# Kernel tuning notes

Hardware: AMD Instinct MI355X
Metric: run time of the kernel (lower is better)

Reference implementation:

```python
import jax, jax.numpy as jnp
import numpy as np

DIM = 576
HEADS = 8
AGENT = 49
GRID_SIZE = 5
ORDER = 3
BN_EPS = 1e-5


def _kan_grid():
    h = 2.0 / GRID_SIZE  # grid_range [-1, 1]
    return jnp.arange(-ORDER, GRID_SIZE + ORDER + 1, dtype=jnp.float32) * h - 1.0


def _bsplines(x, grid):
    # x: (M, in) -> (M, in, GRID_SIZE + ORDER) Cox-de Boor B-spline bases (efficient-kan)
    xe = x[..., None]
    b = ((xe >= grid[:-1]) & (xe < grid[1:])).astype(x.dtype)
    for k in range(1, ORDER + 1):
        b = ((xe - grid[:-(k + 1)]) / (grid[k:-1] - grid[:-(k + 1)]) * b[..., :-1]
             + (grid[k + 1:] - xe) / (grid[k + 1:] - grid[1:-k]) * b[..., 1:])
    return b


def setup_inputs() -> dict:
    key = jax.random.key(0)
    ks = jax.random.split(key, 16)
    b, H, W = 32, 28, 28
    n, c = H * W, DIM
    nrm = lambda k, shape, std=0.02: jax.random.normal(k, shape, jnp.float32) * std
    return {
        "x": jax.random.normal(ks[0], (b, n, c), jnp.float32),
        "H": H,
        "W": W,
        "Wq": nrm(ks[1], (c, c)),
        "Wkv": nrm(ks[2], (2 * c, c)),
        "an_bias": nrm(ks[3], (HEADS, AGENT, 7, 7)),
        "na_bias": nrm(ks[4], (HEADS, AGENT, 7, 7)),
        "ah_bias": nrm(ks[5], (1, HEADS, AGENT, H, 1)),
        "aw_bias": nrm(ks[6], (1, HEADS, AGENT, 1, W)),
        "ha_bias": nrm(ks[7], (1, HEADS, H, 1, AGENT)),
        "wa_bias": nrm(ks[8], (1, HEADS, 1, W, AGENT)),
        "dwc_w": nrm(ks[9], (c, 1, 3, 3), 0.1),
        "dwc_b": jnp.zeros((c,), jnp.float32),
        "bn_gamma": jnp.ones((c,), jnp.float32),
        "bn_beta": jnp.zeros((c,), jnp.float32),
        "bn_mean": jnp.zeros((c,), jnp.float32),
        "bn_var": jnp.ones((c,), jnp.float32),
        "base_weight": nrm(ks[10], (c, c)),
        "spline_weight": nrm(ks[11], (c, c, GRID_SIZE + ORDER)),
        "spline_scaler": jnp.ones((c, c), jnp.float32),
    }


def reference(x, H, W, Wq, Wkv, an_bias, na_bias, ah_bias, aw_bias, ha_bias, wa_bias,
              dwc_w, dwc_b, bn_gamma, bn_beta, bn_mean, bn_var,
              base_weight, spline_weight, spline_scaler):
    b, n, c = x.shape
    h, hd = HEADS, c // HEADS
    scale = hd ** -0.5
    q = x @ Wq.T                       # (b,n,c)
    kv = x @ Wkv.T                     # (b,n,2c)  (sr_ratio == 1)
    k, v = kv[..., :c], kv[..., c:]
    # agent tokens: AdaptiveAvgPool2d(28x28 -> 7x7) == exact 4x4 mean pooling
    p = int(AGENT ** 0.5)
    agent = q.reshape(b, p, H // p, p, W // p, c).mean(axis=(2, 4)).reshape(b, AGENT, c)
    qh = q.reshape(b, n, h, hd).transpose(0, 2, 1, 3)       # (b,h,n,hd)
    kh = k.reshape(b, n, h, hd).transpose(0, 2, 1, 3)
    vh = v.reshape(b, n, h, hd).transpose(0, 2, 1, 3)
    ah = agent.reshape(b, AGENT, h, hd).transpose(0, 2, 1, 3)  # (b,h,A,hd)
    # stage 1: agent tokens attend to k/v (bilinear-upsampled 7x7 bias + separable bias)
    pb1 = jax.image.resize(an_bias, (h, AGENT, H, W), "bilinear").reshape(1, h, AGENT, n)
    pb2 = (ah_bias + aw_bias).reshape(1, h, AGENT, n)
    agent_attn = jax.nn.softmax(jnp.einsum("bhad,bhnd->bhan", ah * scale, kh) + pb1 + pb2, axis=-1)
    agent_v = jnp.einsum("bhan,bhnd->bhad", agent_attn, vh)    # (b,h,A,hd)
    # stage 2: queries attend to agent tokens
    ab1 = jax.image.resize(na_bias, (h, AGENT, H, W), "bilinear").reshape(1, h, AGENT, n).transpose(0, 1, 3, 2)
    ab2 = (ha_bias + wa_bias).reshape(1, h, n, AGENT)
    q_attn = jax.nn.softmax(jnp.einsum("bhnd,bhad->bhna", qh * scale, ah) + ab1 + ab2, axis=-1)
    out = jnp.einsum("bhna,bhad->bhnd", q_attn, agent_v).transpose(0, 2, 1, 3).reshape(b, n, c)
    # depthwise-conv + BN(eval) + ReLU residual on v
    vimg = v.transpose(0, 2, 1).reshape(b, c, H, W)
    y = jax.lax.conv_general_dilated(vimg, dwc_w, (1, 1), "SAME",
                                     feature_group_count=c,
                                     dimension_numbers=("NCHW", "OIHW", "NCHW"))
    y = y + dwc_b[None, :, None, None]
    scale_bn = (bn_gamma / jnp.sqrt(bn_var + BN_EPS))[None, :, None, None]
    y = (y - bn_mean[None, :, None, None]) * scale_bn + bn_beta[None, :, None, None]
    y = jax.nn.relu(y).reshape(b, c, n).transpose(0, 2, 1)
    out = out + y
    # KANLinear projection: silu base branch + B-spline branch
    xf = out.reshape(b * n, c)
    bases = _bsplines(xf, _kan_grid())                           # (M, in, 8)
    scaled = spline_weight * spline_scaler[..., None]            # (out, in, 8)
    proj = jax.nn.silu(xf) @ base_weight.T + jnp.einsum("mik,oik->mo", bases, scaled)
    return proj.reshape(b, n, c)
```

## Files before the change

### kernel.cpp

```cpp
#include <hip/hip_runtime.h>
#include <hip/hip_bf16.h>
#include <math.h>

#define B_ 32
#define N_ 784
#define C_ 576
#define H_ 28
#define W_ 28
#define HEADS_ 8
#define HD_ 72
#define AGENT_ 49
#define M_ (B_ * N_)
#define KTOT_ 5184
#define QKVW_ 1728
#define SCALE_ 0.11785113019775793f
#define LDA_ 40

typedef unsigned short ushort_t;
typedef __attribute__((ext_vector_type(8))) unsigned short u16x8;
typedef __attribute__((ext_vector_type(8))) __bf16 bf16x8;
typedef __attribute__((ext_vector_type(4))) float f32x4;
typedef __attribute__((ext_vector_type(4))) unsigned u32x4;

__device__ __forceinline__ ushort_t f2bf(float f) {
  union { float f; unsigned u; } v; v.f = f;
  unsigned r = v.u + 0x7fffu + ((v.u >> 16) & 1u);
  return (ushort_t)(r >> 16);
}
__device__ __forceinline__ float bf2f(ushort_t u) {
  union { unsigned u; float f; } v; v.u = ((unsigned)u) << 16;
  return v.f;
}
__device__ __forceinline__ unsigned pack2(float lo, float hi) {
  __bf16 a = (__bf16)lo, b = (__bf16)hi;
  unsigned short ua = __builtin_bit_cast(unsigned short, a);
  unsigned short ub = __builtin_bit_cast(unsigned short, b);
  return (unsigned)ua | ((unsigned)ub << 16);
}

__global__ __launch_bounds__(256) void convert_x_kernel(
    const float* __restrict__ x, ushort_t* __restrict__ xbf) {
  const int total8 = M_ * C_ / 8;
  for (int i = blockIdx.x * 256 + threadIdx.x; i < total8; i += gridDim.x * 256) {
    f32x4 a = *(const f32x4*)(x + i * 8);
    f32x4 b = *(const f32x4*)(x + i * 8 + 4);
    u16x8 o;
    o[0]=f2bf(a[0]); o[1]=f2bf(a[1]); o[2]=f2bf(a[2]); o[3]=f2bf(a[3]);
    o[4]=f2bf(b[0]); o[5]=f2bf(b[1]); o[6]=f2bf(b[2]); o[7]=f2bf(b[3]);
    *(u16x8*)(xbf + i * 8) = o;
  }
}

__global__ __launch_bounds__(256) void pack_w_kernel(
    const float* __restrict__ Wq, const float* __restrict__ Wkv,
    ushort_t* __restrict__ wbf) {
  int total = QKVW_ * C_;
  for (int i = blockIdx.x * 256 + threadIdx.x; i < total; i += gridDim.x * 256) {
    int j = i / C_, k = i % C_;
    float v = (j < C_) ? Wq[(size_t)j * C_ + k] : Wkv[(size_t)(j - C_) * C_ + k];
    wbf[i] = f2bf(v);
  }
}

__global__ __launch_bounds__(256) void pack_b_kernel(
    const float* __restrict__ base_w, const float* __restrict__ spline_w,
    const float* __restrict__ spline_s, ushort_t* __restrict__ bpackb) {
  int o = blockIdx.x;
  for (int j = threadIdx.x; j < KTOT_; j += 256) {
    float v;
    if (j < C_) {
      v = base_w[(size_t)o * C_ + j];
    } else {
      int jj = j - C_;
      int i = jj >> 3, kk = jj & 7;
      v = spline_w[((size_t)o * C_ + i) * 8 + kk] * spline_s[(size_t)o * C_ + i];
    }
    bpackb[(size_t)o * KTOT_ + j] = f2bf(v);
  }
}

__device__ __forceinline__ float bilerp7(const float* __restrict__ Bsrc, int y, int x) {
  float sy = y * 0.25f - 0.375f;
  float sx = x * 0.25f - 0.375f;
  float fy0 = floorf(sy), fx0 = floorf(sx);
  int y0 = (int)fy0, x0 = (int)fx0;
  float fy = sy - fy0, fx = sx - fx0;
  int y0c = min(6, max(0, y0)), y1c = min(6, max(0, y0 + 1));
  int x0c = min(6, max(0, x0)), x1c = min(6, max(0, x0 + 1));
  float v00 = Bsrc[y0c * 7 + x0c], v01 = Bsrc[y0c * 7 + x1c];
  float v10 = Bsrc[y1c * 7 + x0c], v11 = Bsrc[y1c * 7 + x1c];
  return (1.f - fy) * ((1.f - fx) * v00 + fx * v01)
       + fy * ((1.f - fx) * v10 + fx * v11);
}

__global__ __launch_bounds__(256) void bias_kernel(
    const float* __restrict__ an_bias, const float* __restrict__ na_bias,
    const float* __restrict__ ah_bias, const float* __restrict__ aw_bias,
    const float* __restrict__ ha_bias, const float* __restrict__ wa_bias,
    float* __restrict__ abias, float* __restrict__ qbias) {
  int idx = blockIdx.x * 256 + threadIdx.x;
  if (idx >= HEADS_ * AGENT_ * N_) return;
  int n = idx % N_;
  int ha = idx / N_;
  int h = ha / AGENT_, a = ha % AGENT_;
  int y = n / W_, x = n % W_;
  float pb1 = bilerp7(an_bias + (size_t)ha * 49, y, x);
  float pb2 = ah_bias[ha * H_ + y] + aw_bias[ha * W_ + x];
  abias[(size_t)ha * N_ + n] = pb1 + pb2;
  float ab1 = bilerp7(na_bias + (size_t)ha * 49, y, x);
  float ab2 = ha_bias[(h * H_ + y) * AGENT_ + a] + wa_bias[(h * W_ + x) * AGENT_ + a];
  qbias[((size_t)h * N_ + n) * AGENT_ + a] = ab1 + ab2;
}

__global__ __launch_bounds__(256, 2) void mfma_qkv_kernel(
    const ushort_t* __restrict__ A, const ushort_t* __restrict__ Bt,
    ushort_t* __restrict__ out) {
  __shared__ ushort_t Asl[2][128 * LDA_];
  __shared__ ushort_t Bsl[2][192 * LDA_];
  const int tid = threadIdx.x;
  const int lane = tid & 63, wid = tid >> 6;
  const int wm = wid >> 1, wn = wid & 1;
  const int m0 = blockIdx.y * 128, n0 = blockIdx.x * 192;
  const int l16 = lane & 15, lq = lane >> 4;

  const int rA = tid >> 1, hA = tid & 1;
  int rB[3], cB[3];
  #pragma unroll
  for (int u = 0; u < 3; ++u) { int it = tid + u * 256; rB[u] = it >> 2; cB[u] = it & 3; }

  const ushort_t* arow = A + (size_t)(m0 + rA) * C_ + hA * 16;

  f32x4 acc[4][6] = {};
  u16x8 ar0, ar1, br[3];

  ar0 = *(const u16x8*)(arow + 0);
  ar1 = *(const u16x8*)(arow + 8);
  #pragma unroll
  for (int u = 0; u < 3; ++u)
    br[u] = *(const u16x8*)(Bt + (size_t)(n0 + rB[u]) * C_ + cB[u] * 8);
  *(u16x8*)&Asl[0][rA * LDA_ + hA * 16] = ar0;
  *(u16x8*)&Asl[0][rA * LDA_ + hA * 16 + 8] = ar1;
  #pragma unroll
  for (int u = 0; u < 3; ++u) *(u16x8*)&Bsl[0][rB[u] * LDA_ + cB[u] * 8] = br[u];
  ar0 = *(const u16x8*)(arow + 32);
  ar1 = *(const u16x8*)(arow + 40);
  #pragma unroll
  for (int u = 0; u < 3; ++u)
    br[u] = *(const u16x8*)(Bt + (size_t)(n0 + rB[u]) * C_ + 32 + cB[u] * 8);
  __syncthreads();

  const int NSTEP = C_ / 32;
  for (int s = 0; s < NSTEP; ++s) {
    const int cur = s & 1;
    bf16x8 af[4], bfr[6];
    #pragma unroll
    for (int fm = 0; fm < 4; ++fm)
      af[fm] = *(const bf16x8*)&Asl[cur][(wm * 64 + fm * 16 + l16) * LDA_ + lq * 8];
    #pragma unroll
    for (int fn = 0; fn < 6; ++fn)
      bfr[fn] = *(const bf16x8*)&Bsl[cur][(wn * 96 + fn * 16 + l16) * LDA_ + lq * 8];
    #pragma unroll
    for (int fm = 0; fm < 4; ++fm)
      #pragma unroll
      for (int fn = 0; fn < 6; ++fn)
        acc[fm][fn] = __builtin_amdgcn_mfma_f32_16x16x32_bf16(
            af[fm], bfr[fn], acc[fm][fn], 0, 0, 0);
    if (s + 1 < NSTEP) {
      const int nxt = cur ^ 1;
      *(u16x8*)&Asl[nxt][rA * LDA_ + hA * 16] = ar0;
      *(u16x8*)&Asl[nxt][rA * LDA_ + hA * 16 + 8] = ar1;
      #pragma unroll
      for (int u = 0; u < 3; ++u) *(u16x8*)&Bsl[nxt][rB[u] * LDA_ + cB[u] * 8] = br[u];
      if (s + 2 < NSTEP) {
        const int kl = (s + 2) * 32;
        ar0 = *(const u16x8*)(arow + kl);
        ar1 = *(const u16x8*)(arow + kl + 8);
        #pragma unroll
        for (int u = 0; u < 3; ++u)
          br[u] = *(const u16x8*)(Bt + (size_t)(n0 + rB[u]) * C_ + kl + cB[u] * 8);
      }
    }
    __syncthreads();
  }
  #pragma unroll
  for (int fm = 0; fm < 4; ++fm) {
    #pragma unroll
    for (int fn = 0; fn < 6; ++fn) {
      int col = n0 + wn * 96 + fn * 16 + l16;
      #pragma unroll
      for (int r = 0; r < 4; ++r) {
        int row = m0 + wm * 64 + fm * 16 + lq * 4 + r;
        out[(size_t)row * QKVW_ + col] = f2bf(acc[fm][fn][r]);
      }
    }
  }
}

__device__ __forceinline__ u32x4 basesPack(float xv) {
  float s = __fmaf_rn(xv, 2.5f, 5.5f);
  float tf = floorf(s);
  int t = (int)tf;
  float u = s - tf;
  float u2 = u * u, u3 = u2 * u, um = 1.f - u;
  float p0 = u3 * (1.f / 6.f);
  float p1 = (-3.f * u3 + 3.f * u2 + 3.f * u + 1.f) * (1.f / 6.f);
  float p2 = (3.f * u3 - 6.f * u2 + 4.f) * (1.f / 6.f);
  float p3 = um * um * um * (1.f / 6.f);
  unsigned lo = pack2(p3, p2);
  unsigned hi = pack2(p1, p0);
  unsigned cm1 = lo << 16;
  unsigned c1  = (lo >> 16) | (hi << 16);
  unsigned c3  = hi >> 16;
  bool inr = (t >= 0) && (t <= 10);
  u32x4 o;
  #pragma unroll
  for (int j = 0; j < 4; ++j) {
    int d = 3 - t + 2 * j;
    unsigned r = 0u;
    r = (d == -1) ? cm1 : r;
    r = (d == 0)  ? lo  : r;
    r = (d == 1)  ? c1  : r;
    r = (d == 2)  ? hi  : r;
    r = (d == 3)  ? c3  : r;
    o[j] = inr ? r : 0u;
  }
  return o;
}

__device__ __forceinline__ u32x4 siluPack(const float* xv) {
  u32x4 o;
  #pragma unroll
  for (int e = 0; e < 4; ++e) {
    float v0 = xv[2 * e], v1 = xv[2 * e + 1];
    float s0 = v0 / (1.f + __expf(-v0));
    float s1 = v1 / (1.f + __expf(-v1));
    o[e] = pack2(s0, s1);
  }
  return o;
}

__global__ __launch_bounds__(256, 2) void kan_mfma_kernel(
    const float* __restrict__ xf, const ushort_t* __restrict__ Bt,
    float* __restrict__ out) {
  __shared__ ushort_t Asl[2][128 * LDA_];
  __shared__ ushort_t Bsl[2][192 * LDA_];
  const int tid = threadIdx.x;
  const int lane = tid & 63, wid = tid >> 6;
  const int wm = wid >> 1, wn = wid & 1;
  const int m0 = blockIdx.y * 128, n0 = blockIdx.x * 192;
  const int l16 = lane & 15, lq = lane >> 4;

  const int rA = tid >> 1, hA = tid & 1;
  int rB[3], cB[3];
  #pragma unroll
  for (int u = 0; u < 3; ++u) { int it = tid + u * 256; rB[u] = it >> 2; cB[u] = it & 3; }

  const float* xfr = xf + (size_t)(m0 + rA) * C_;

  f32x4 acc[4][6] = {};
  float xv[16];
  u16x8 br[3];

  #pragma unroll
  for (int q = 0; q < 4; ++q) {
    f32x4 t4 = *(const f32x4*)(xfr + hA * 16 + q * 4);
    xv[q * 4 + 0] = t4[0]; xv[q * 4 + 1] = t4[1];
    xv[q * 4 + 2] = t4[2]; xv[q * 4 + 3] = t4[3];
  }
  #pragma unroll
  for (int u = 0; u < 3; ++u)
    br[u] = *(const u16x8*)(Bt + (size_t)(n0 + rB[u]) * KTOT_ + cB[u] * 8);
  {
    u32x4 a0 = siluPack(xv), a1 = siluPack(xv + 8);
    *(u32x4*)&Asl[0][rA * LDA_ + hA * 16] = a0;
    *(u32x4*)&Asl[0][rA * LDA_ + hA * 16 + 8] = a1;
    #pragma unroll
    for (int u = 0; u < 3; ++u) *(u16x8*)&Bsl[0][rB[u] * LDA_ + cB[u] * 8] = br[u];
  }
  #pragma unroll
  for (int q = 0; q < 4; ++q) {
    f32x4 t4 = *(const f32x4*)(xfr + 32 + hA * 16 + q * 4);
    xv[q * 4 + 0] = t4[0]; xv[q * 4 + 1] = t4[1];
    xv[q * 4 + 2] = t4[2]; xv[q * 4 + 3] = t4[3];
  }
  #pragma unroll
  for (int u = 0; u < 3; ++u)
    br[u] = *(const u16x8*)(Bt + (size_t)(n0 + rB[u]) * KTOT_ + 32 + cB[u] * 8);
  __syncthreads();

  const int NSTEP = KTOT_ / 32;
  for (int s = 0; s < NSTEP; ++s) {
    const int cur = s & 1;
    bf16x8 af[4], bfr[6];
    #pragma unroll
    for (int fm = 0; fm < 4; ++fm)
      af[fm] = *(const bf16x8*)&Asl[cur][(wm * 64 + fm * 16 + l16) * LDA_ + lq * 8];
    #pragma unroll
    for (int fn = 0; fn < 6; ++fn)
      bfr[fn] = *(const bf16x8*)&Bsl[cur][(wn * 96 + fn * 16 + l16) * LDA_ + lq * 8];
    #pragma unroll
    for (int fm = 0; fm < 4; ++fm)
      #pragma unroll
      for (int fn = 0; fn < 6; ++fn)
        acc[fm][fn] = __builtin_amdgcn_mfma_f32_16x16x32_bf16(
            af[fm], bfr[fn], acc[fm][fn], 0, 0, 0);
    if (s + 1 < NSTEP) {
      const int nxt = cur ^ 1;
      const int kg = (s + 1) * 32;
      u32x4 a0, a1;
      if (kg < C_) { a0 = siluPack(xv); a1 = siluPack(xv + 8); }
      else         { a0 = basesPack(xv[0]); a1 = basesPack(xv[1]); }
      *(u32x4*)&Asl[nxt][rA * LDA_ + hA * 16] = a0;
      *(u32x4*)&Asl[nxt][rA * LDA_ + hA * 16 + 8] = a1;
      #pragma unroll
      for (int u = 0; u < 3; ++u) *(u16x8*)&Bsl[nxt][rB[u] * LDA_ + cB[u] * 8] = br[u];
      if (s + 2 < NSTEP) {
        const int kl = (s + 2) * 32;
        if (kl < C_) {
          #pragma unroll
          for (int q = 0; q < 4; ++q) {
            f32x4 t4 = *(const f32x4*)(xfr + kl + hA * 16 + q * 4);
            xv[q * 4 + 0] = t4[0]; xv[q * 4 + 1] = t4[1];
            xv[q * 4 + 2] = t4[2]; xv[q * 4 + 3] = t4[3];
          }
        } else {
          int i0 = ((kl - C_) >> 3) + hA * 2;
          xv[0] = xfr[i0];
          xv[1] = xfr[i0 + 1];
        }
        #pragma unroll
        for (int u = 0; u < 3; ++u)
          br[u] = *(const u16x8*)(Bt + (size_t)(n0 + rB[u]) * KTOT_ + kl + cB[u] * 8);
      }
    }
    __syncthreads();
  }
  #pragma unroll
  for (int fm = 0; fm < 4; ++fm) {
    #pragma unroll
    for (int fn = 0; fn < 6; ++fn) {
      int col = n0 + wn * 96 + fn * 16 + l16;
      #pragma unroll
      for (int r = 0; r < 4; ++r) {
        int row = m0 + wm * 64 + fm * 16 + lq * 4 + r;
        out[(size_t)row * C_ + col] = acc[fm][fn][r];
      }
    }
  }
}

__global__ __launch_bounds__(576) void agent_pool_kernel(
    const ushort_t* __restrict__ qkvb, float* __restrict__ agent) {
  int ba = blockIdx.x;
  int b = ba / AGENT_, a = ba % AGENT_;
  int ay = a / 7, ax = a % 7;
  int ch = threadIdx.x;
  float s = 0.f;
  #pragma unroll
  for (int i2 = 0; i2 < 4; ++i2)
    #pragma unroll
    for (int i4 = 0; i4 < 4; ++i4)
      s += bf2f(qkvb[((size_t)b * N_ + (ay * 4 + i2) * W_ + (ax * 4 + i4)) * QKVW_ + ch]);
  agent[(size_t)ba * C_ + ch] = s * 0.0625f;
}

#define AKS_ 104
#define VTS_ 136
__global__ __launch_bounds__(256) void agent_attn_mfma_kernel(
    const float* __restrict__ agent, const ushort_t* __restrict__ qkvb,
    const float* __restrict__ abias, float* __restrict__ agent_v) {
  __shared__ ushort_t A_lds[64 * AKS_];
  __shared__ ushort_t K_lds[112 * AKS_];
  __shared__ ushort_t Vt_lds[80 * VTS_];
  __shared__ ushort_t P_lds[4][16 * VTS_];
  const int tid = threadIdx.x;
  const int lane = tid & 63, wid = tid >> 6;
  const int l16 = lane & 15, lq = lane >> 4;
  const int b = blockIdx.x >> 3, h = blockIdx.x & 7;

  for (int i = tid; i < 64 * AKS_; i += 256) A_lds[i] = 0;
  for (int i = tid; i < 112 * 32; i += 256) {
    int r = i >> 5, cc = 72 + (i & 31);
    K_lds[r * AKS_ + cc] = 0;
  }
  for (int i = tid; i < 80 * VTS_; i += 256) Vt_lds[i] = 0;
  for (int i = tid; i < 4 * 16 * 24; i += 256) {
    int w = i / (16 * 24), rest = i % (16 * 24);
    int r = rest / 24, cc = 112 + rest % 24;
    P_lds[w][r * VTS_ + cc] = 0;
  }
  for (int i = tid; i < AGENT_ * HD_; i += 256) {
    int a = i / HD_, d = i % HD_;
    A_lds[a * AKS_ + d] = f2bf(agent[((size_t)b * AGENT_ + a) * C_ + h * HD_ + d]);
  }

  int srow[4], scol[4]; bool sval[4];
  #pragma unroll
  for (int i = 0; i < 4; ++i) {
    int idx = tid + i * 256;
    srow[i] = idx / 9; scol[i] = idx % 9;
    sval[i] = idx < 1008;
  }
  const ushort_t* kbase = qkvb + (size_t)b * N_ * QKVW_ + C_ + h * HD_;
  const ushort_t* vbase = qkvb + (size_t)b * N_ * QKVW_ + 2 * C_ + h * HD_;

  u16x8 kreg[4], vreg[4];
  #pragma unroll
  for (int i = 0; i < 4; ++i) {
    if (sval[i]) {
      kreg[i] = *(const u16x8*)(kbase + (size_t)srow[i] * QKVW_ + scol[i] * 8);
      vreg[i] = *(const u16x8*)(vbase + (size_t)srow[i] * QKVW_ + scol[i] * 8);
    }
  }
  #pragma unroll
  for (int i = 0; i < 4; ++i) {
    if (sval[i]) {
      *(u16x8*)&K_lds[srow[i] * AKS_ + scol[i] * 8] = kreg[i];
      #pragma unroll
      for (int e = 0; e < 8; ++e)
        Vt_lds[(scol[i] * 8 + e) * VTS_ + srow[i]] = vreg[i][e];
    }
  }
  __syncthreads();

  float m_r[4] = {-1e30f, -1e30f, -1e30f, -1e30f};
  float l_r[4] = {};
  f32x4 O[5] = {};
  const float* bias_base[4];
  #pragma unroll
  for (int r = 0; r < 4; ++r) {
    int a = wid * 16 + lq * 4 + r;
    a = min(a, AGENT_ - 1);
    bias_base[r] = abias + ((size_t)h * AGENT_ + a) * N_;
  }

  for (int c = 0; c < 7; ++c) {
    if (c < 6) {
      const size_t off = (size_t)(c + 1) * 112 * QKVW_;
      #pragma unroll
      for (int i = 0; i < 4; ++i) {
        if (sval[i]) {
          kreg[i] = *(const u16x8*)(kbase + off + (size_t)srow[i] * QKVW_ + scol[i] * 8);
          vreg[i] = *(const u16x8*)(vbase + off + (size_t)srow[i] * QKVW_ + scol[i] * 8);
        }
      }
    }
    f32x4 sacc[7] = {};
    #pragma unroll
    for (int ks = 0; ks < 3; ++ks) {
      bf16x8 af = *(const bf16x8*)&A_lds[(wid * 16 + l16) * AKS_ + ks * 32 + lq * 8];
      #pragma unroll
      for (int nt = 0; nt < 7; ++nt) {
        bf16x8 bf = *(const bf16x8*)&K_lds[(nt * 16 + l16) * AKS_ + ks * 32 + lq * 8];
        sacc[nt] = __builtin_amdgcn_mfma_f32_16x16x32_bf16(af, bf, sacc[nt], 0, 0, 0);
      }
    }
    float cmax[4] = {-1e30f, -1e30f, -1e30f, -1e30f};
    const int nb = c * 112 + l16;
    #pragma unroll
    for (int nt = 0; nt < 7; ++nt)
      #pragma unroll
      for (int r = 0; r < 4; ++r) {
        float lg = sacc[nt][r] * SCALE_ + bias_base[r][nb + nt * 16];
        sacc[nt][r] = lg;
        cmax[r] = fmaxf(cmax[r], lg);
      }
    #pragma unroll
    for (int off = 1; off < 16; off <<= 1)
      #pragma unroll
      for (int r = 0; r < 4; ++r)
        cmax[r] = fmaxf(cmax[r], __shfl_xor(cmax[r], off));
    float scl[4], rs[4];
    #pragma unroll
    for (int r = 0; r < 4; ++r) {
      float nm = fmaxf(m_r[r], cmax[r]);
      scl[r] = __expf(m_r[r] - nm);
      m_r[r] = nm;
      rs[r] = 0.f;
    }
    #pragma unroll
    for (int nt = 0; nt < 7; ++nt)
      #pragma unroll
      for (int r = 0; r < 4; ++r) {
        float p = __expf(sacc[nt][r] - m_r[r]);
        rs[r] += p;
        P_lds[wid][(lq * 4 + r) * VTS_ + nt * 16 + l16] = f2bf(p);
      }
    #pragma unroll
    for (int off = 1; off < 16; off <<= 1)
      #pragma unroll
      for (int r = 0; r < 4; ++r)
        rs[r] += __shfl_xor(rs[r], off);
    #pragma unroll
    for (int r = 0; r < 4; ++r) l_r[r] = l_r[r] * scl[r] + rs[r];
    #pragma unroll
    for (int nt = 0; nt < 5; ++nt)
      #pragma unroll
      for (int r = 0; r < 4; ++r) O[nt][r] *= scl[r];
    #pragma unroll
    for (int ks = 0; ks < 4; ++ks) {
      bf16x8 pf = *(const bf16x8*)&P_lds[wid][l16 * VTS_ + ks * 32 + lq * 8];
      #pragma unroll
      for (int nt = 0; nt < 5; ++nt) {
        bf16x8 vf = *(const bf16x8*)&Vt_lds[(nt * 16 + l16) * VTS_ + ks * 32 + lq * 8];
        O[nt] = __builtin_amdgcn_mfma_f32_16x16x32_bf16(pf, vf, O[nt], 0, 0, 0);
      }
    }
    __syncthreads();
    if (c < 6) {
      #pragma unroll
      for (int i = 0; i < 4; ++i) {
        if (sval[i]) {
          *(u16x8*)&K_lds[srow[i] * AKS_ + scol[i] * 8] = kreg[i];
          #pragma unroll
          for (int e = 0; e < 8; ++e)
            Vt_lds[(scol[i] * 8 + e) * VTS_ + srow[i]] = vreg[i][e];
        }
      }
      __syncthreads();
    }
  }
  float inv[4];
  #pragma unroll
  for (int r = 0; r < 4; ++r) inv[r] = 1.f / l_r[r];
  #pragma unroll
  for (int nt = 0; nt < 5; ++nt) {
    int d = nt * 16 + l16;
    if (d >= HD_) continue;
    #pragma unroll
    for (int r = 0; r < 4; ++r) {
      int a = wid * 16 + lq * 4 + r;
      if (a < AGENT_)
        agent_v[(((size_t)b * HEADS_ + h) * AGENT_ + a) * HD_ + d] = O[nt][r] * inv[r];
    }
  }
}

__global__ __launch_bounds__(256) void q_attn_kernel(
    const ushort_t* __restrict__ qkvb, const float* __restrict__ agent,
    const float* __restrict__ agent_v, const float* __restrict__ qbias,
    float* __restrict__ xf) {
  __shared__ float ag_t[HD_ * 52];
  __shared__ float av_t[HD_ * 52];
  const int tid = threadIdx.x;
  const int h = blockIdx.y, b = blockIdx.z;
  for (int t = tid; t < AGENT_ * HD_; t += 256) {
    int a = t / HD_, d = t % HD_;
    ag_t[d * 52 + a] = agent[((size_t)b * AGENT_ + a) * C_ + h * HD_ + d];
    av_t[d * 52 + a] = agent_v[(((size_t)b * HEADS_ + h) * AGENT_ + a) * HD_ + d];
  }
  __syncthreads();
  const int n = blockIdx.x * 256 + tid;
  if (n >= N_) return;
  const ushort_t* qp = qkvb + ((size_t)b * N_ + n) * QKVW_ + h * HD_;
  const float* qb = qbias + ((size_t)h * N_ + n) * AGENT_;
  float lg[AGENT_];
  #pragma unroll
  for (int a = 0; a < AGENT_; ++a) lg[a] = qb[a];
  for (int d = 0; d < HD_; ++d) {
    float qd = bf2f(qp[d]) * SCALE_;
    #pragma unroll
    for (int a = 0; a < AGENT_; ++a) lg[a] += qd * ag_t[d * 52 + a];
  }
  float mx = -1e30f;
  #pragma unroll
  for (int a = 0; a < AGENT_; ++a) mx = fmaxf(mx, lg[a]);
  float s = 0.f;
  #pragma unroll
  for (int a = 0; a < AGENT_; ++a) { lg[a] = __expf(lg[a] - mx); s += lg[a]; }
  float inv = 1.f / s;
  #pragma unroll
  for (int a = 0; a < AGENT_; ++a) lg[a] *= inv;
  float* op = xf + ((size_t)b * N_ + n) * C_ + h * HD_;
  for (int d = 0; d < HD_; ++d) {
    float acc = 0.f;
    #pragma unroll
    for (int a = 0; a < AGENT_; ++a) acc += lg[a] * av_t[d * 52 + a];
    op[d] = acc;
  }
}

__global__ __launch_bounds__(288) void dwc_kernel(
    const ushort_t* __restrict__ qkvb, const float* __restrict__ w,
    const float* __restrict__ bias, const float* __restrict__ gamma,
    const float* __restrict__ beta, const float* __restrict__ mean,
    const float* __restrict__ var, float* __restrict__ xf) {
  const int bn = blockIdx.x;
  const int b = bn / N_, n = bn % N_;
  const int y = n / W_, x = n % W_;
  const int c0 = threadIdx.x * 2;
  float a0 = 0.f, a1 = 0.f;
  #pragma unroll
  for (int ky = 0; ky < 3; ++ky) {
    int yy = y + ky - 1;
    if (yy < 0 || yy >= H_) continue;
    #pragma unroll
    for (int kx = 0; kx < 3; ++kx) {
      int xx = x + kx - 1;
      if (xx < 0 || xx >= W_) continue;
      unsigned v = *(const unsigned*)(qkvb + ((size_t)b * N_ + yy * W_ + xx) * QKVW_ + 2 * C_ + c0);
      a0 += w[c0 * 9 + ky * 3 + kx] * bf2f((ushort_t)(v & 0xffffu));
      a1 += w[(c0 + 1) * 9 + ky * 3 + kx] * bf2f((ushort_t)(v >> 16));
    }
  }
  float s0 = gamma[c0] * rsqrtf(var[c0] + 1e-5f);
  float s1 = gamma[c0 + 1] * rsqrtf(var[c0 + 1] + 1e-5f);
  float r0 = fmaxf((a0 + bias[c0] - mean[c0]) * s0 + beta[c0], 0.f);
  float r1 = fmaxf((a1 + bias[c0 + 1] - mean[c0 + 1]) * s1 + beta[c0 + 1], 0.f);
  float2* xp = (float2*)&xf[(size_t)bn * C_ + c0];
  float2 old = *xp;
  old.x += r0; old.y += r1;
  *xp = old;
}

extern "C" void kernel_launch(void* const* d_in, const int* in_sizes, int n_in,
                              void* d_out, int out_size, void* d_ws, size_t ws_size,
                              hipStream_t stream) {
  const float* x        = (const float*)d_in[0];
  const float* Wq       = (const float*)d_in[3];
  const float* Wkv      = (const float*)d_in[4];
  const float* an_bias  = (const float*)d_in[5];
  const float* na_bias  = (const float*)d_in[6];
  const float* ah_bias  = (const float*)d_in[7];
  const float* aw_bias  = (const float*)d_in[8];
  const float* ha_bias  = (const float*)d_in[9];
  const float* wa_bias  = (const float*)d_in[10];
  const float* dwc_w    = (const float*)d_in[11];
  const float* dwc_b    = (const float*)d_in[12];
  const float* bn_gamma = (const float*)d_in[13];
  const float* bn_beta  = (const float*)d_in[14];
  const float* bn_mean  = (const float*)d_in[15];
  const float* bn_var   = (const float*)d_in[16];
  const float* base_w   = (const float*)d_in[17];
  const float* spline_w = (const float*)d_in[18];
  const float* spline_s = (const float*)d_in[19];

  char* ws = (char*)d_ws;
  ushort_t* qkvb   = (ushort_t*)(ws + 0);
  ushort_t* xbf    = (ushort_t*)(ws + 86704128);
  ushort_t* wbf    = (ushort_t*)(ws + 115605504);
  ushort_t* bpackb = (ushort_t*)(ws + 117596160);
  float* agent     = (float*)(ws + 123568128);
  float* agent_v   = (float*)(ws + 127180800);
  float* abias     = (float*)(ws + 130793472);
  float* qbias     = (float*)(ws + 132022784);
  float* xf        = (float*)(ws + 133252096);
  float* out       = (float*)d_out;

  convert_x_kernel<<<dim3(2048), dim3(256), 0, stream>>>(x, xbf);
  pack_w_kernel<<<dim3(1024), dim3(256), 0, stream>>>(Wq, Wkv, wbf);
  pack_b_kernel<<<dim3(C_), dim3(256), 0, stream>>>(base_w, spline_w, spline_s, bpackb);
  bias_kernel<<<dim3((HEADS_ * AGENT_ * N_ + 255) / 256), dim3(256), 0, stream>>>(
      an_bias, na_bias, ah_bias, aw_bias, ha_bias, wa_bias, abias, qbias);
  mfma_qkv_kernel<<<dim3(9, 196), dim3(256), 0, stream>>>(xbf, wbf, qkvb);
  agent_pool_kernel<<<dim3(B_ * AGENT_), dim3(C_), 0, stream>>>(qkvb, agent);
  agent_attn_mfma_kernel<<<dim3(B_ * HEADS_), dim3(256), 0, stream>>>(
      agent, qkvb, abias, agent_v);
  q_attn_kernel<<<dim3(4, HEADS_, B_), dim3(256), 0, stream>>>(
      qkvb, agent, agent_v, qbias, xf);
  dwc_kernel<<<dim3(M_), dim3(288), 0, stream>>>(
      qkvb, dwc_w, dwc_b, bn_gamma, bn_beta, bn_mean, bn_var, xf);
  kan_mfma_kernel<<<dim3(3, 196), dim3(256), 0, stream>>>(xf, bpackb, out);
}
```

Baseline: 721.2 us.

## Use 8-warp blocks and XCD-aware tile remapping in both MFMA GEMMs

Both the QKV GEMM and the KAN GEMM now launch 512-thread blocks (8 wavefronts) on the same 128x192 tile, so each wave computes a 64x48 sub-tile and fewer accumulators per thread. The 2D grid becomes a 1D grid whose block index is remapped so that consecutive tiles land on the same XCD, aiming for better L2 reuse of the shared A/B rows. The goal is more waves per CU to hide latency and better cache locality. The cost is extra index arithmetic, half the threads idle for the second B load, and more LDS-read traffic per MFMA because each wave now has a smaller tile.

```diff
diff --git a/kernel.cpp b/kernel.cpp
--- a/kernel.cpp
+++ b/kernel.cpp
@@ -112,72 +112,71 @@
   qbias[((size_t)h * N_ + n) * AGENT_ + a] = ab1 + ab2;
 }
 
-__global__ __launch_bounds__(256, 2) void mfma_qkv_kernel(
+__global__ __launch_bounds__(512, 4) void mfma_qkv_kernel(
     const ushort_t* __restrict__ A, const ushort_t* __restrict__ Bt,
     ushort_t* __restrict__ out) {
   __shared__ ushort_t Asl[2][128 * LDA_];
   __shared__ ushort_t Bsl[2][192 * LDA_];
   const int tid = threadIdx.x;
   const int lane = tid & 63, wid = tid >> 6;
-  const int wm = wid >> 1, wn = wid & 1;
-  const int m0 = blockIdx.y * 128, n0 = blockIdx.x * 192;
+  const int wm = wid >> 2, wn = wid & 3;
   const int l16 = lane & 15, lq = lane >> 4;
 
-  const int rA = tid >> 1, hA = tid & 1;
-  int rB[3], cB[3];
-  #pragma unroll
-  for (int u = 0; u < 3; ++u) { int it = tid + u * 256; rB[u] = it >> 2; cB[u] = it & 3; }
-
-  const ushort_t* arow = A + (size_t)(m0 + rA) * C_ + hA * 16;
-
-  f32x4 acc[4][6] = {};
-  u16x8 ar0, ar1, br[3];
-
-  ar0 = *(const u16x8*)(arow + 0);
-  ar1 = *(const u16x8*)(arow + 8);
-  #pragma unroll
-  for (int u = 0; u < 3; ++u)
-    br[u] = *(const u16x8*)(Bt + (size_t)(n0 + rB[u]) * C_ + cB[u] * 8);
-  *(u16x8*)&Asl[0][rA * LDA_ + hA * 16] = ar0;
-  *(u16x8*)&Asl[0][rA * LDA_ + hA * 16 + 8] = ar1;
-  #pragma unroll
-  for (int u = 0; u < 3; ++u) *(u16x8*)&Bsl[0][rB[u] * LDA_ + cB[u] * 8] = br[u];
-  ar0 = *(const u16x8*)(arow + 32);
-  ar1 = *(const u16x8*)(arow + 40);
-  #pragma unroll
-  for (int u = 0; u < 3; ++u)
-    br[u] = *(const u16x8*)(Bt + (size_t)(n0 + rB[u]) * C_ + 32 + cB[u] * 8);
+  int lin = blockIdx.x;
+  const int q = 220, r = 4;
+  int xcd = lin & 7;
+  int wg = (xcd < r ? xcd * (q + 1) : r * (q + 1) + (xcd - r) * q) + (lin >> 3);
+  const int m0 = (wg / 9) * 128, n0 = (wg % 9) * 192;
+
+  const int rA = tid >> 2, hA = tid & 3;
+  const int rB0 = tid >> 2, cB0 = tid & 3;
+  const int rB1 = 128 + (tid >> 2), cB1 = tid & 3;
+  const bool hasB1 = tid < 256;
+
+  const ushort_t* arow = A + (size_t)(m0 + rA) * C_ + hA * 8;
+  const ushort_t* brow0 = Bt + (size_t)(n0 + rB0) * C_ + cB0 * 8;
+  const ushort_t* brow1 = Bt + (size_t)(n0 + rB1) * C_ + cB1 * 8;
+
+  f32x4 acc[4][3] = {};
+  u16x8 ar, br0, br1;
+
+  ar = *(const u16x8*)(arow);
+  br0 = *(const u16x8*)(brow0);
+  if (hasB1) br1 = *(const u16x8*)(brow1);
+  *(u16x8*)&Asl[0][rA * LDA_ + hA * 8] = ar;
+  *(u16x8*)&Bsl[0][rB0 * LDA_ + cB0 * 8] = br0;
+  if (hasB1) *(u16x8*)&Bsl[0][rB1 * LDA_ + cB1 * 8] = br1;
+  ar = *(const u16x8*)(arow + 32);
+  br0 = *(const u16x8*)(brow0 + 32);
+  if (hasB1) br1 = *(const u16x8*)(brow1 + 32);
   __syncthreads();
 
   const int NSTEP = C_ / 32;
   for (int s = 0; s < NSTEP; ++s) {
     const int cur = s & 1;
-    bf16x8 af[4], bfr[6];
+    bf16x8 af[4], bfr[3];
     #pragma unroll
     for (int fm = 0; fm < 4; ++fm)
       af[fm] = *(const bf16x8*)&Asl[cur][(wm * 64 + fm * 16 + l16) * LDA_ + lq * 8];
     #pragma unroll
-    for (int fn = 0; fn < 6; ++fn)
-      bfr[fn] = *(const bf16x8*)&Bsl[cur][(wn * 96 + fn * 16 + l16) * LDA_ + lq * 8];
+    for (int fn = 0; fn < 3; ++fn)
+      bfr[fn] = *(const bf16x8*)&Bsl[cur][(wn * 48 + fn * 16 + l16) * LDA_ + lq * 8];
     #pragma unroll
     for (int fm = 0; fm < 4; ++fm)
       #pragma unroll
-      for (int fn = 0; fn < 6; ++fn)
+      for (int fn = 0; fn < 3; ++fn)
         acc[fm][fn] = __builtin_amdgcn_mfma_f32_16x16x32_bf16(
             af[fm], bfr[fn], acc[fm][fn], 0, 0, 0);
     if (s + 1 < NSTEP) {
       const int nxt = cur ^ 1;
-      *(u16x8*)&Asl[nxt][rA * LDA_ + hA * 16] = ar0;
-      *(u16x8*)&Asl[nxt][rA * LDA_ + hA * 16 + 8] = ar1;
-      #pragma unroll
-      for (int u = 0; u < 3; ++u) *(u16x8*)&Bsl[nxt][rB[u] * LDA_ + cB[u] * 8] = br[u];
+      *(u16x8*)&Asl[nxt][rA * LDA_ + hA * 8] = ar;
+      *(u16x8*)&Bsl[nxt][rB0 * LDA_ + cB0 * 8] = br0;
+      if (hasB1) *(u16x8*)&Bsl[nxt][rB1 * LDA_ + cB1 * 8] = br1;
       if (s + 2 < NSTEP) {
         const int kl = (s + 2) * 32;
-        ar0 = *(const u16x8*)(arow + kl);
-        ar1 = *(const u16x8*)(arow + kl + 8);
-        #pragma unroll
-        for (int u = 0; u < 3; ++u)
-          br[u] = *(const u16x8*)(Bt + (size_t)(n0 + rB[u]) * C_ + kl + cB[u] * 8);
+        ar = *(const u16x8*)(arow + kl);
+        br0 = *(const u16x8*)(brow0 + kl);
+        if (hasB1) br1 = *(const u16x8*)(brow1 + kl);
       }
     }
     __syncthreads();
@@ -185,12 +184,12 @@
   #pragma unroll
   for (int fm = 0; fm < 4; ++fm) {
     #pragma unroll
-    for (int fn = 0; fn < 6; ++fn) {
-      int col = n0 + wn * 96 + fn * 16 + l16;
-      #pragma unroll
-      for (int r = 0; r < 4; ++r) {
-        int row = m0 + wm * 64 + fm * 16 + lq * 4 + r;
-        out[(size_t)row * QKVW_ + col] = f2bf(acc[fm][fn][r]);
+    for (int fn = 0; fn < 3; ++fn) {
+      int col = n0 + wn * 48 + fn * 16 + l16;
+      #pragma unroll
+      for (int r2 = 0; r2 < 4; ++r2) {
+        int row = m0 + wm * 64 + fm * 16 + lq * 4 + r2;
+        out[(size_t)row * QKVW_ + col] = f2bf(acc[fm][fn][r2]);
       }
     }
   }
@@ -216,13 +215,13 @@
   #pragma unroll
   for (int j = 0; j < 4; ++j) {
     int d = 3 - t + 2 * j;
-    unsigned r = 0u;
-    r = (d == -1) ? cm1 : r;
-    r = (d == 0)  ? lo  : r;
-    r = (d == 1)  ? c1  : r;
-    r = (d == 2)  ? hi  : r;
-    r = (d == 3)  ? c3  : r;
-    o[j] = inr ? r : 0u;
+    unsigned rr = 0u;
+    rr = (d == -1) ? cm1 : rr;
+    rr = (d == 0)  ? lo  : rr;
+    rr = (d == 1)  ? c1  : rr;
+    rr = (d == 2)  ? hi  : rr;
+    rr = (d == 3)  ? c3  : rr;
+    o[j] = inr ? rr : 0u;
   }
   return o;
 }
@@ -239,98 +238,91 @@
   return o;
 }
 
-__global__ __launch_bounds__(256, 2) void kan_mfma_kernel(
+__global__ __launch_bounds__(512, 4) void kan_mfma_kernel(
     const float* __restrict__ xf, const ushort_t* __restrict__ Bt,
     float* __restrict__ out) {
   __shared__ ushort_t Asl[2][128 * LDA_];
   __shared__ ushort_t Bsl[2][192 * LDA_];
   const int tid = threadIdx.x;
   const int lane = tid & 63, wid = tid >> 6;
-  const int wm = wid >> 1, wn = wid & 1;
-  const int m0 = blockIdx.y * 128, n0 = blockIdx.x * 192;
+  const int wm = wid >> 2, wn = wid & 3;
   const int l16 = lane & 15, lq = lane >> 4;
 
-  const int rA = tid >> 1, hA = tid & 1;
-  int rB[3], cB[3];
-  #pragma unroll
-  for (int u = 0; u < 3; ++u) { int it = tid + u * 256; rB[u] = it >> 2; cB[u] = it & 3; }
+  int lin = blockIdx.x;
+  const int q = 73, r = 4;
+  int xcd = lin & 7;
+  int wg = (xcd < r ? xcd * (q + 1) : r * (q + 1) + (xcd - r) * q) + (lin >> 3);
+  const int m0 = (wg / 3) * 128, n0 = (wg % 3) * 192;
+
+  const int rA = tid >> 2, hA = tid & 3;
+  const int rB0 = tid >> 2, cB0 = tid & 3;
+  const int rB1 = 128 + (tid >> 2), cB1 = tid & 3;
+  const bool hasB1 = tid < 256;
 
   const float* xfr = xf + (size_t)(m0 + rA) * C_;
-
-  f32x4 acc[4][6] = {};
-  float xv[16];
-  u16x8 br[3];
-
-  #pragma unroll
-  for (int q = 0; q < 4; ++q) {
-    f32x4 t4 = *(const f32x4*)(xfr + hA * 16 + q * 4);
-    xv[q * 4 + 0] = t4[0]; xv[q * 4 + 1] = t4[1];
-    xv[q * 4 + 2] = t4[2]; xv[q * 4 + 3] = t4[3];
-  }
-  #pragma unroll
-  for (int u = 0; u < 3; ++u)
-    br[u] = *(const u16x8*)(Bt + (size_t)(n0 + rB[u]) * KTOT_ + cB[u] * 8);
+  const ushort_t* brow0 = Bt + (size_t)(n0 + rB0) * KTOT_ + cB0 * 8;
+  const ushort_t* brow1 = Bt + (size_t)(n0 + rB1) * KTOT_ + cB1 * 8;
+
+  f32x4 acc[4][3] = {};
+  float xv[8];
+  u16x8 br0, br1;
+
   {
-    u32x4 a0 = siluPack(xv), a1 = siluPack(xv + 8);
-    *(u32x4*)&Asl[0][rA * LDA_ + hA * 16] = a0;
-    *(u32x4*)&Asl[0][rA * LDA_ + hA * 16 + 8] = a1;
-    #pragma unroll
-    for (int u = 0; u < 3; ++u) *(u16x8*)&Bsl[0][rB[u] * LDA_ + cB[u] * 8] = br[u];
-  }
-  #pragma unroll
-  for (int q = 0; q < 4; ++q) {
-    f32x4 t4 = *(const f32x4*)(xfr + 32 + hA * 16 + q * 4);
-    xv[q * 4 + 0] = t4[0]; xv[q * 4 + 1] = t4[1];
-    xv[q * 4 + 2] = t4[2]; xv[q * 4 + 3] = t4[3];
-  }
-  #pragma unroll
-  for (int u = 0; u < 3; ++u)
-    br[u] = *(const u16x8*)(Bt + (size_t)(n0 + rB[u]) * KTOT_ + 32 + cB[u] * 8);
+    f32x4 a = *(const f32x4*)(xfr + hA * 8);
+    f32x4 b = *(const f32x4*)(xfr + hA * 8 + 4);
+    xv[0]=a[0]; xv[1]=a[1]; xv[2]=a[2]; xv[3]=a[3];
+    xv[4]=b[0]; xv[5]=b[1]; xv[6]=b[2]; xv[7]=b[3];
+  }
+  br0 = *(const u16x8*)(brow0);
+  if (hasB1) br1 = *(const u16x8*)(brow1);
+  *(u32x4*)&Asl[0][rA * LDA_ + hA * 8] = siluPack(xv);
+  *(u16x8*)&Bsl[0][rB0 * LDA_ + cB0 * 8] = br0;
+  if (hasB1) *(u16x8*)&Bsl[0][rB1 * LDA_ + cB1 * 8] = br1;
+  {
+    f32x4 a = *(const f32x4*)(xfr + 32 + hA * 8);
+    f32x4 b = *(const f32x4*)(xfr + 32 + hA * 8 + 4);
+    xv[0]=a[0]; xv[1]=a[1]; xv[2]=a[2]; xv[3]=a[3];
+    xv[4]=b[0]; xv[5]=b[1]; xv[6]=b[2]; xv[7]=b[3];
+  }
+  br0 = *(const u16x8*)(brow0 + 32);
+  if (hasB1) br1 = *(const u16x8*)(brow1 + 32);
   __syncthreads();
 
   const int NSTEP = KTOT_ / 32;
   for (int s = 0; s < NSTEP; ++s) {
     const int cur = s & 1;
-    bf16x8 af[4], bfr[6];
+    bf16x8 af[4], bfr[3];
     #pragma unroll
     for (int fm = 0; fm < 4; ++fm)
       af[fm] = *(const bf16x8*)&Asl[cur][(wm * 64 + fm * 16 + l16) * LDA_ + lq * 8];
     #pragma unroll
-    for (int fn = 0; fn < 6; ++fn)
-      bfr[fn] = *(const bf16x8*)&Bsl[cur][(wn * 96 + fn * 16 + l16) * LDA_ + lq * 8];
+    for (int fn = 0; fn < 3; ++fn)
+      bfr[fn] = *(const bf16x8*)&Bsl[cur][(wn * 48 + fn * 16 + l16) * LDA_ + lq * 8];
     #pragma unroll
     for (int fm = 0; fm < 4; ++fm)
       #pragma unroll
-      for (int fn = 0; fn < 6; ++fn)
+      for (int fn = 0; fn < 3; ++fn)
         acc[fm][fn] = __builtin_amdgcn_mfma_f32_16x16x32_bf16(
             af[fm], bfr[fn], acc[fm][fn], 0, 0, 0);
     if (s + 1 < NSTEP) {
       const int nxt = cur ^ 1;
       const int kg = (s + 1) * 32;
-      u32x4 a0, a1;
-      if (kg < C_) { a0 = siluPack(xv); a1 = siluPack(xv + 8); }
-      else         { a0 = basesPack(xv[0]); a1 = basesPack(xv[1]); }
-      *(u32x4*)&Asl[nxt][rA * LDA_ + hA * 16] = a0;
-      *(u32x4*)&Asl[nxt][rA * LDA_ + hA * 16 + 8] = a1;
-      #pragma unroll
-      for (int u = 0; u < 3; ++u) *(u16x8*)&Bsl[nxt][rB[u] * LDA_ + cB[u] * 8] = br[u];
+      u32x4 a0 = (kg < C_) ? siluPack(xv) : basesPack(xv[0]);
+      *(u32x4*)&Asl[nxt][rA * LDA_ + hA * 8] = a0;
+      *(u16x8*)&Bsl[nxt][rB0 * LDA_ + cB0 * 8] = br0;
+      if (hasB1) *(u16x8*)&Bsl[nxt][rB1 * LDA_ + cB1 * 8] = br1;
       if (s + 2 < NSTEP) {
         const int kl = (s + 2) * 32;
         if (kl < C_) {
-          #pragma unroll
-          for (int q = 0; q < 4; ++q) {
-            f32x4 t4 = *(const f32x4*)(xfr + kl + hA * 16 + q * 4);
-            xv[q * 4 + 0] = t4[0]; xv[q * 4 + 1] = t4[1];
-            xv[q * 4 + 2] = t4[2]; xv[q * 4 + 3] = t4[3];
-          }
+          f32x4 a = *(const f32x4*)(xfr + kl + hA * 8);
+          f32x4 b = *(const f32x4*)(xfr + kl + hA * 8 + 4);
+          xv[0]=a[0]; xv[1]=a[1]; xv[2]=a[2]; xv[3]=a[3];
+          xv[4]=b[0]; xv[5]=b[1]; xv[6]=b[2]; xv[7]=b[3];
         } else {
-          int i0 = ((kl - C_) >> 3) + hA * 2;
-          xv[0] = xfr[i0];
-          xv[1] = xfr[i0 + 1];
+          xv[0] = xfr[((kl - C_) >> 3) + hA];
         }
-        #pragma unroll
-        for (int u = 0; u < 3; ++u)
-          br[u] = *(const u16x8*)(Bt + (size_t)(n0 + rB[u]) * KTOT_ + kl + cB[u] * 8);
+        br0 = *(const u16x8*)(brow0 + kl);
+        if (hasB1) br1 = *(const u16x8*)(brow1 + kl);
       }
     }
     __syncthreads();
@@ -338,12 +330,12 @@
   #pragma unroll
   for (int fm = 0; fm < 4; ++fm) {
     #pragma unroll
-    for (int fn = 0; fn < 6; ++fn) {
-      int col = n0 + wn * 96 + fn * 16 + l16;
-      #pragma unroll
-      for (int r = 0; r < 4; ++r) {
-        int row = m0 + wm * 64 + fm * 16 + lq * 4 + r;
-        out[(size_t)row * C_ + col] = acc[fm][fn][r];
+    for (int fn = 0; fn < 3; ++fn) {
+      int col = n0 + wn * 48 + fn * 16 + l16;
+      #pragma unroll
+      for (int r2 = 0; r2 < 4; ++r2) {
+        int row = m0 + wm * 64 + fm * 16 + lq * 4 + r2;
+        out[(size_t)row * C_ + col] = acc[fm][fn][r2];
       }
     }
   }
@@ -652,7 +644,7 @@
   pack_b_kernel<<<dim3(C_), dim3(256), 0, stream>>>(base_w, spline_w, spline_s, bpackb);
   bias_kernel<<<dim3((HEADS_ * AGENT_ * N_ + 255) / 256), dim3(256), 0, stream>>>(
       an_bias, na_bias, ah_bias, aw_bias, ha_bias, wa_bias, abias, qbias);
-  mfma_qkv_kernel<<<dim3(9, 196), dim3(256), 0, stream>>>(xbf, wbf, qkvb);
+  mfma_qkv_kernel<<<dim3(1764), dim3(512), 0, stream>>>(xbf, wbf, qkvb);
   agent_pool_kernel<<<dim3(B_ * AGENT_), dim3(C_), 0, stream>>>(qkvb, agent);
   agent_attn_mfma_kernel<<<dim3(B_ * HEADS_), dim3(256), 0, stream>>>(
       agent, qkvb, abias, agent_v);
@@ -660,5 +652,5 @@
       qkvb, agent, agent_v, qbias, xf);
   dwc_kernel<<<dim3(M_), dim3(288), 0, stream>>>(
       qkvb, dwc_w, dwc_b, bn_gamma, bn_beta, bn_mean, bn_var, xf);
-  kan_mfma_kernel<<<dim3(3, 196), dim3(256), 0, stream>>>(xf, bpackb, out);
-}
+  kan_mfma_kernel<<<dim3(588), dim3(512), 0, stream>>>(xf, bpackb, out);
+}
```

Measured after the change: 672.0 us. 1.07x faster.
